# Kernel optimization log

Hardware: AMD Instinct MI355X
Metric: run time of the kernel (lower is better)

Reference implementation:

```python
import jax, jax.numpy as jnp
import numpy as np

V, E, H, OUT = 32000, 256, 256, 32000
B, TE, TD = 16, 128, 64


def gru_layer(x, h0, Wih, Whh, bih, bhh, lengths):
    """PyTorch-semantics GRU over padded batch-first x:(B,T,I), h0:(B,H).
    Emulates pack/pad: hidden frozen and output zeroed past each sample's length."""
    T = x.shape[1]

    def step(h, inp):
        xt, t = inp  # xt:(B,I)
        gi = xt @ Wih.T + bih          # (B,3H)
        gh = h @ Whh.T + bhh
        ir, iz, inn = jnp.split(gi, 3, axis=-1)
        hr, hz, hn = jnp.split(gh, 3, axis=-1)
        r = jax.nn.sigmoid(ir + hr)
        z = jax.nn.sigmoid(iz + hz)
        n = jnp.tanh(inn + r * hn)
        hnew = (1.0 - z) * n + z * h
        valid = (t < lengths)[:, None]
        h = jnp.where(valid, hnew, h)
        out = jnp.where(valid, hnew, 0.0)
        return h, out

    hT, ys = jax.lax.scan(step, h0, (jnp.swapaxes(x, 0, 1), jnp.arange(T)))
    return jnp.swapaxes(ys, 0, 1), hT  # (B,T,H), (B,H)


def setup_inputs() -> dict:
    key = jax.random.key(0)
    ks = jax.random.split(key, 20)
    s = 0.05
    enc_len = jax.random.randint(ks[0], (B,), 1, TE + 1).at[0].set(TE)
    dec_len = jax.random.randint(ks[1], (B,), 1, TD + 1).at[0].set(TD)
    return {
        "encoder_input": jax.random.randint(ks[2], (B, TE), 0, V),
        "encoder_length": enc_len,
        "decoder_input": jax.random.randint(ks[3], (B, TD), 0, V),
        "decoder_length": dec_len,
        "embedding": jax.random.normal(ks[4], (V, E)) * s,
        "enc_Wih": jax.random.normal(ks[5], (3 * H, E)) * s,
        "enc_Whh": jax.random.normal(ks[6], (3 * H, H)) * s,
        "enc_bih": jax.random.normal(ks[7], (3 * H,)) * s,
        "enc_bhh": jax.random.normal(ks[8], (3 * H,)) * s,
        "dec_Wih": jax.random.normal(ks[9], (3 * H, E)) * s,
        "dec_Whh": jax.random.normal(ks[10], (3 * H, H)) * s,
        "dec_bih": jax.random.normal(ks[11], (3 * H,)) * s,
        "dec_bhh": jax.random.normal(ks[12], (3 * H,)) * s,
        "attn_W": jax.random.normal(ks[13], (H, 2 * H)) * s,
        "attn_Wb": jnp.zeros((H,)),
        "attn_v": jax.random.normal(ks[14], (1, H)) * s,
        "attn_vb": jnp.zeros((1,)),
        "dense_W": jax.random.normal(ks[15], (H, 2 * H)) * s,
        "dense_b": jnp.zeros((H,)),
        "out_W": jax.random.normal(ks[16], (OUT, H)) * s,
        "out_b": jnp.zeros((OUT,)),
    }


def reference(encoder_input, encoder_length, decoder_input, decoder_length,
              embedding, enc_Wih, enc_Whh, enc_bih, enc_bhh,
              dec_Wih, dec_Whh, dec_bih, dec_bhh,
              attn_W, attn_Wb, attn_v, attn_vb,
              dense_W, dense_b, out_W, out_b):
    enc_x = embedding[encoder_input]  # (B,TE,E)
    dec_x = embedding[decoder_input]  # (B,TD,E)

    h0 = jnp.zeros((B, H), dtype=enc_x.dtype)
    enc_out, enc_h = gru_layer(enc_x, h0, enc_Wih, enc_Whh, enc_bih, enc_bhh, encoder_length)
    dec_out, _ = gru_layer(dec_x, enc_h, dec_Wih, dec_Whh, dec_bih, dec_bhh, decoder_length)

    # --- additive attention with per-sample length mask ---
    enc_valid = jnp.arange(TE) < encoder_length[:, None]     # (B,TE)
    dec_valid = jnp.arange(TD) < decoder_length[:, None]     # (B,TD)
    mask = (dec_valid[:, :, None] & enc_valid[:, None, :]).astype(enc_out.dtype)[..., None]  # (B,TD,TE,1)

    enc_e = enc_out[:, None, :, :] * mask  # (B,TD,TE,H)
    dec_e = dec_out[:, :, None, :] * mask  # (B,TD,TE,H)

    score = jnp.tanh(jnp.concatenate([enc_e, dec_e], axis=3) @ attn_W.T + attn_Wb)
    energy = score @ attn_v.T + attn_vb  # (B,TD,TE,1)
    a = jax.nn.softmax(energy, axis=2)   # softmax over encoder steps (unmasked, as original)
    aw = a * mask
    s = aw.sum(axis=2)                   # (B,TD,1)
    s = jnp.where(s == 0, 1.0, s)
    attention = aw / s[:, :, None, :]
    context = (attention * enc_e).sum(axis=2)  # (B,TD,H); dropout is identity (eval)

    outputs = jnp.concatenate([dec_out, context], axis=2)  # (B,TD,2H)
    dense = jnp.tanh(outputs @ dense_W.T + dense_b)
    logits = dense @ out_W.T + out_b  # (B,TD,OUT)
    return logits
```

## Files before the change

### kernel.cpp

```cpp
#include <hip/hip_runtime.h>
#include <hip/hip_bf16.h>

typedef unsigned short ushort_t;
typedef unsigned int uint_t;
typedef unsigned long long u64_t;

#define BB 16
#define TE 128
#define TD 64
#define HH 256
#define G3 768
#define KK 256
#define OUTV 32000
#define MROWS_E (BB*TE)
#define MROWS_D (BB*TD)
#define NBLK 16
#define JD 16
#define QW_PER_BUF 2048

typedef __attribute__((ext_vector_type(8))) short short8;
typedef __attribute__((ext_vector_type(4))) float f32x4;

__device__ __forceinline__ float b2f(ushort_t u) {
  union { uint_t i; float f; } v; v.i = ((uint_t)u) << 16; return v.f;
}
__device__ __forceinline__ ushort_t f2b(float f) {
  union { float f; uint_t i; } v; v.f = f;
  uint_t x = v.i;
  return (ushort_t)((x + 0x7fffu + ((x >> 16) & 1u)) >> 16);
}
__device__ __forceinline__ float ldf(const void* p, size_t i, uint_t f32f) {
  return f32f ? ((const float*)p)[i] : b2f(((const ushort_t*)p)[i]);
}
__device__ __forceinline__ float fsig(float x) { return 1.f/(1.f + __expf(-x)); }
__device__ __forceinline__ float ftanh(float x) { return 1.f - 2.f/(__expf(2.f*x) + 1.f); }

__global__ __launch_bounds__(256) void detect_kernel(const void* emb, uint_t* flag) {
  int tid = threadIdx.x;
  uint_t w = ((const uint_t*)emb)[tid];
  uint_t e = (w >> 7) & 0xFFu;
  bool pass = (e >= 100u && e <= 127u);
  unsigned long long m = __ballot(pass);
  __shared__ int cnt[4];
  if ((tid & 63) == 0) cnt[tid >> 6] = __popcll(m);
  __syncthreads();
  if (tid == 0) {
    int c = cnt[0] + cnt[1] + cnt[2] + cnt[3];
    *flag = (c >= 128) ? 0u : 1u;
  }
}

__global__ __launch_bounds__(256) void prep_kernel(
    const void* eWhh, const void* dWhh, const void* denseW,
    const void* ebih, const void* ebhh, const void* dbih, const void* dbhh,
    const void* outb, const uint_t* flagp,
    ushort_t* WBe, ushort_t* WBd, ushort_t* DWT,
    float* cbe, float* cbd, float* obf, u64_t* hq) {
  uint_t f = *flagp;
  int tid = blockIdx.x * blockDim.x + threadIdx.x;
  int nth = gridDim.x * blockDim.x;
  for (int i = tid; i < G3*KK; i += nth) {
    WBe[i] = f2b(ldf(eWhh, i, f));
    WBd[i] = f2b(ldf(dWhh, i, f));
  }
  for (int i = tid; i < 512*HH; i += nth) {
    int k = i / HH, c = i % HH;
    DWT[i] = f2b(ldf(denseW, (size_t)c*512 + k, f));
  }
  for (int i = tid; i < G3; i += nth) {
    float be = ldf(ebih, i, f), bd = ldf(dbih, i, f);
    if (i < 2*HH) { be += ldf(ebhh, i, f); bd += ldf(dbhh, i, f); }
    cbe[i] = be; cbd[i] = bd;
  }
  for (int i = tid; i < OUTV; i += nth) obf[i] = ldf(outb, i, f);
  for (int i = tid; i < 2*QW_PER_BUF; i += nth) hq[i] = 0ull;
}

#define LDT 264

__global__ __launch_bounds__(256) void gemm_kernel(
    const ushort_t* A, const int* tokens, const void* emb,
    const void* Bw, int ldb, int b_off,
    const float* bias, const uint_t* flagp,
    float* Cf, ushort_t* Cb, int ldc, int M, int tshift, int a_f32) {
  __shared__ __align__(16) ushort_t Bs[64*LDT];
  __shared__ __align__(16) ushort_t As[32*LDT];
  uint_t f = *flagp;
  int tid = threadIdx.x;
  int wave = tid >> 6, lane = tid & 63;
  int n0 = blockIdx.x * 64;
#pragma unroll
  for (int it = 0; it < 8; ++it) {
    int idx = it*256 + tid;
    int row = idx >> 5, col = (idx & 31) << 3;
    size_t e = (size_t)(n0 + row)*ldb + col + b_off;
    uint4 v;
    if (f) {
      const float4* s = (const float4*)((const float*)Bw + e);
      float4 x = s[0], y = s[1];
      v.x = (uint_t)f2b(x.x) | ((uint_t)f2b(x.y) << 16);
      v.y = (uint_t)f2b(x.z) | ((uint_t)f2b(x.w) << 16);
      v.z = (uint_t)f2b(y.x) | ((uint_t)f2b(y.y) << 16);
      v.w = (uint_t)f2b(y.z) | ((uint_t)f2b(y.w) << 16);
    } else {
      v = *(const uint4*)((const ushort_t*)Bw + e);
    }
    *(uint4*)(Bs + row*LDT + col) = v;
  }
  int arow_i = lane & 15;
  float bias_v = 0.f;
  if (bias) bias_v = bias[n0 + wave*16 + arow_i];
  int koff = (lane >> 4) << 3;
  for (int m0 = blockIdx.y*32; m0 < M; m0 += gridDim.y*32) {
    __syncthreads();
#pragma unroll
    for (int it = 0; it < 4; ++it) {
      int idx = it*256 + tid;
      int row = idx >> 5, col = (idx & 31) << 3;
      uint4 v;
      if (tokens) {
        size_t e = (size_t)tokens[m0 + row]*KK + col;
        if (f) {
          const float4* s = (const float4*)((const float*)emb + e);
          float4 x = s[0], y = s[1];
          v.x = (uint_t)f2b(x.x) | ((uint_t)f2b(x.y) << 16);
          v.y = (uint_t)f2b(x.z) | ((uint_t)f2b(x.w) << 16);
          v.z = (uint_t)f2b(y.x) | ((uint_t)f2b(y.y) << 16);
          v.w = (uint_t)f2b(y.z) | ((uint_t)f2b(y.w) << 16);
        } else {
          v = *(const uint4*)((const ushort_t*)emb + e);
        }
      } else if (a_f32) {
        const float4* s = (const float4*)((const float*)A + (size_t)(m0 + row)*KK + col);
        float4 x = s[0], y = s[1];
        v.x = (uint_t)f2b(x.x) | ((uint_t)f2b(x.y) << 16);
        v.y = (uint_t)f2b(x.z) | ((uint_t)f2b(x.w) << 16);
        v.z = (uint_t)f2b(y.x) | ((uint_t)f2b(y.y) << 16);
        v.w = (uint_t)f2b(y.z) | ((uint_t)f2b(y.w) << 16);
      } else {
        v = *(const uint4*)(A + (size_t)(m0 + row)*KK + col);
      }
      *(uint4*)(As + row*LDT + col) = v;
    }
    __syncthreads();
#pragma unroll
    for (int msub = 0; msub < 2; ++msub) {
      f32x4 acc = {0.f,0.f,0.f,0.f};
      const ushort_t* ap = As + (msub*16 + arow_i)*LDT + koff;
      const ushort_t* bp = Bs + (wave*16 + arow_i)*LDT + koff;
#pragma unroll
      for (int ks = 0; ks < 8; ++ks) {
        short8 af = *(const short8*)(ap + ks*32);
        short8 bf = *(const short8*)(bp + ks*32);
        acc = __builtin_amdgcn_mfma_f32_16x16x32_bf16(af, bf, acc, 0, 0, 0);
      }
      int mbase = m0 + msub*16 + (lane >> 4)*4;
      int ncol = n0 + wave*16 + arow_i;
#pragma unroll
      for (int r = 0; r < 4; ++r) {
        float val = acc[r] + bias_v;
        int mr = mbase + r;
        int orow = tshift ? (((mr & ((1 << tshift) - 1)) << 4) + (mr >> tshift)) : mr;
        if (Cf) Cf[(size_t)orow*ldc + ncol] = val;
        else    Cb[(size_t)orow*ldc + ncol] = f2b(val);
      }
    }
  }
}

#define HSBF 264

__device__ __forceinline__ void stage_w(const ushort_t* WB, int j0, int tid,
                                        ushort_t* wlds) {
#pragma unroll
  for (int it = 0; it < 6; ++it) {
    int idx = it*256 + tid;
    int row = idx >> 5, col = (idx & 31) << 3;
    const ushort_t* src = WB + ((size_t)((row >> 4)*HH + j0 + (row & 15)))*KK + col;
    *(uint4*)(wlds + row*HSBF + col) = *(const uint4*)src;
  }
}

__global__ __launch_bounds__(256) void gru_kernel(
    const float* gi_e, const float* gi_d, const ushort_t* WBe, const ushort_t* WBd,
    const void* ebhh, const void* dbhh, const uint_t* flagp,
    const int* elen, const int* dlen, float* eout, float* dout, u64_t* hq) {
  uint_t f = *flagp;
  __shared__ __align__(16) ushort_t wlds[48*HSBF];
  __shared__ __align__(16) float part[2][4][3][16][17];
  const int tid = threadIdx.x;
  const int wave = tid >> 6, lane = tid & 63;
  const int mrow = lane & 15, quad = lane >> 4;
  const int j0 = blockIdx.x * JD;
  const int m = tid >> 4, n = tid & 15;
  const int j = j0 + n;
  const int je = j & ~1;
  const int widx = ((je >> 6) << 9) + (((je >> 5) & 1) << 8)
                 + (((je >> 1) & 3) << 6) + (((je >> 3) & 3) << 4) + m;

  stage_w(WBe, j0, tid, wlds);
  const float bn_e = ldf(ebhh, 2*HH + j, f);
  const float bn_d = ldf(dbhh, 2*HH + j, f);
  const int len_e = elen[m], len_d = dlen[m];
  float hreg = 0.f;
  float grv = gi_e[(size_t)m*G3 + j];
  float gzv = gi_e[(size_t)m*G3 + HH + j];
  float gnv = gi_e[(size_t)m*G3 + 2*HH + j];
  __syncthreads();

  for (int s = 0; s < TE + TD; ++s) {
    if (s == TE) {
      stage_w(WBd, j0, tid, wlds);
      __syncthreads();
    }
    const bool enc = s < TE;
    const int t = enc ? s : s - TE;
    const u64_t* hbR = hq + (size_t)(s & 1)*QW_PER_BUF + wave*512 + lane;
    u64_t qv[8];
    const uint_t target = (uint_t)s;
    int guard = 0;
    for (;;) {
      bool ok = true;
#pragma unroll
      for (int ks = 0; ks < 2; ++ks)
#pragma unroll
        for (int i = 0; i < 4; ++i) {
          qv[ks*4 + i] = __hip_atomic_load(hbR + ks*256 + i*64,
                                           __ATOMIC_RELAXED, __HIP_MEMORY_SCOPE_AGENT);
          ok = ok && ((uint_t)qv[ks*4 + i] == target);
        }
      if (__all(ok) || ++guard > 30000) break;
    }
    f32x4 ar = {0.f,0.f,0.f,0.f}, az = {0.f,0.f,0.f,0.f}, an = {0.f,0.f,0.f,0.f};
#pragma unroll
    for (int ks = 0; ks < 2; ++ks) {
      union { uint_t u[4]; short8 s8; } av;
#pragma unroll
      for (int i = 0; i < 4; ++i) av.u[i] = (uint_t)(qv[ks*4 + i] >> 32);
      const ushort_t* wp = wlds + mrow*HSBF + wave*64 + ks*32 + quad*8;
      short8 b0 = *(const short8*)(wp);
      short8 b1 = *(const short8*)(wp + 16*HSBF);
      short8 b2 = *(const short8*)(wp + 32*HSBF);
      ar = __builtin_amdgcn_mfma_f32_16x16x32_bf16(av.s8, b0, ar, 0, 0, 0);
      az = __builtin_amdgcn_mfma_f32_16x16x32_bf16(av.s8, b1, az, 0, 0, 0);
      an = __builtin_amdgcn_mfma_f32_16x16x32_bf16(av.s8, b2, an, 0, 0, 0);
    }
    const int p = s & 1;
#pragma unroll
    for (int r = 0; r < 4; ++r) {
      part[p][wave][0][quad*4 + r][mrow] = ar[r];
      part[p][wave][1][quad*4 + r][mrow] = az[r];
      part[p][wave][2][quad*4 + r][mrow] = an[r];
    }
    __syncthreads();
    float accr = 0.f, accz = 0.f, accn = 0.f;
#pragma unroll
    for (int w = 0; w < 4; ++w) {
      accr += part[p][w][0][m][n];
      accz += part[p][w][1][m][n];
      accn += part[p][w][2][m][n];
    }
    float rr = fsig(grv + accr);
    float zz = fsig(gzv + accz);
    float nn = ftanh(gnv + rr*(accn + (enc ? bn_e : bn_d)));
    float hc = (1.f - zz)*nn + zz*hreg;
    bool valid = t < (enc ? len_e : len_d);
    float ov = valid ? hc : 0.f;
    hreg = valid ? hc : hreg;
    if (enc) eout[((size_t)(m*TE + t))*HH + j] = ov;
    else     dout[((size_t)(m*TD + t))*HH + j] = ov;
    uint_t h16 = (uint_t)f2b(hreg);
    uint_t up = (uint_t)__shfl_down((int)h16, 1);
    if (!(n & 1)) {
      u64_t q = ((u64_t)(h16 | (up << 16)) << 32) | (u64_t)(uint_t)(s + 1);
      __hip_atomic_store(hq + (size_t)((s + 1) & 1)*QW_PER_BUF + widx,
                         q, __ATOMIC_RELAXED, __HIP_MEMORY_SCOPE_AGENT);
    }
    int s2 = s + 1;
    if (s2 < TE + TD) {
      const float* g2 = (s2 < TE) ? (gi_e + (size_t)(s2*BB + m)*G3)
                                  : (gi_d + (size_t)((s2 - TE)*BB + m)*G3);
      grv = g2[j]; gzv = g2[HH + j]; gnv = g2[2*HH + j];
    }
  }
}

__global__ __launch_bounds__(256) void attn_kernel(
    const float* eprj, const float* dprj, const float* eout, const float* dout,
    const void* Wb, const void* av, const void* avb,
    const ushort_t* DWT, const void* db, const uint_t* flagp,
    const int* elen, const int* dlen, ushort_t* dense_bf) {
  int bd = blockIdx.x;
  int b = bd / TD, td = bd % TD;
  int tid = threadIdx.x;
  int wave = tid >> 6, lane = tid & 63;
  uint_t f = *flagp;
  __shared__ float dp[HH], dsrow[HH], vv[HH], att[TE];
  int el = elen[b];
  bool dok = td < dlen[b];
  size_t drow = (size_t)bd * HH;
  dp[tid] = dprj[drow + tid] + ldf(Wb, tid, f);
  dsrow[tid] = dout[drow + tid];
  vv[tid] = ldf(av, tid, f);
  if (tid < TE) att[tid] = 0.f;
  __syncthreads();
  float ctx = 0.f;
  if (dok) {
    float vb0 = ldf(avb, 0, f);
    int nteb = (el + 3) >> 2;
    for (int teb = 0; teb < nteb; ++teb) {
      int te = teb*4 + wave;
      if (te < el) {
        const float* ep = eprj + (size_t)(b*TE + te)*HH;
        float s = 0.f;
#pragma unroll
        for (int i = 0; i < 4; ++i) {
          int hh = lane + 64*i;
          s += ftanh(ep[hh] + dp[hh]) * vv[hh];
        }
#pragma unroll
        for (int off = 32; off > 0; off >>= 1) s += __shfl_xor(s, off);
        if (lane == 0) att[te] = s + vb0;
      }
    }
    __syncthreads();
    float mx = -1e30f;
    for (int te = 0; te < el; ++te) mx = fmaxf(mx, att[te]);
    __syncthreads();
    if (tid < el) att[tid] = __expf(att[tid] - mx);
    __syncthreads();
    float ssum = 0.f;
    for (int te = 0; te < el; ++te) ssum += att[te];
    float inv = (ssum > 0.f) ? 1.f/ssum : 0.f;
    const float* ebase = eout + (size_t)(b*TE)*HH + tid;
    float c0 = 0.f, c1 = 0.f, c2 = 0.f, c3 = 0.f;
    int te = 0;
    for (; te + 4 <= el; te += 4) {
      c0 += att[te    ] * ebase[(size_t)(te    )*HH];
      c1 += att[te + 1] * ebase[(size_t)(te + 1)*HH];
      c2 += att[te + 2] * ebase[(size_t)(te + 2)*HH];
      c3 += att[te + 3] * ebase[(size_t)(te + 3)*HH];
    }
    for (; te < el; ++te) c0 += att[te] * ebase[(size_t)te*HH];
    ctx = (c0 + c1 + c2 + c3) * inv;
  }
  __syncthreads();
  dp[tid] = ctx;
  __syncthreads();
  const ushort_t* w0 = DWT + tid;
  float a0 = ldf(db, tid, f), a1 = 0.f, a2 = 0.f, a3 = 0.f;
#pragma unroll 8
  for (int k = 0; k < HH; k += 4) {
    a0 = fmaf(b2f(w0[(size_t)(k    )*HH]), dsrow[k    ], a0);
    a1 = fmaf(b2f(w0[(size_t)(k + 1)*HH]), dsrow[k + 1], a1);
    a2 = fmaf(b2f(w0[(size_t)(k + 2)*HH]), dsrow[k + 2], a2);
    a3 = fmaf(b2f(w0[(size_t)(k + 3)*HH]), dsrow[k + 3], a3);
  }
#pragma unroll 8
  for (int k = 0; k < HH; k += 4) {
    a0 = fmaf(b2f(w0[(size_t)(HH + k    )*HH]), dp[k    ], a0);
    a1 = fmaf(b2f(w0[(size_t)(HH + k + 1)*HH]), dp[k + 1], a1);
    a2 = fmaf(b2f(w0[(size_t)(HH + k + 2)*HH]), dp[k + 2], a2);
    a3 = fmaf(b2f(w0[(size_t)(HH + k + 3)*HH]), dp[k + 3], a3);
  }
  dense_bf[drow + tid] = f2b(ftanh(a0 + a1 + a2 + a3));
}

extern "C" void kernel_launch(void* const* d_in, const int* in_sizes, int n_in,
                              void* d_out, int out_size, void* d_ws, size_t ws_size,
                              hipStream_t stream) {
  const int* enc_in   = (const int*)d_in[0];
  const int* enc_len  = (const int*)d_in[1];
  const int* dec_in   = (const int*)d_in[2];
  const int* dec_len  = (const int*)d_in[3];
  const void* emb    = d_in[4];
  const void* eWih   = d_in[5];
  const void* eWhh   = d_in[6];
  const void* ebih   = d_in[7];
  const void* ebhh   = d_in[8];
  const void* dWih   = d_in[9];
  const void* dWhh   = d_in[10];
  const void* dbih   = d_in[11];
  const void* dbhh   = d_in[12];
  const void* attnW  = d_in[13];
  const void* attnWb = d_in[14];
  const void* attnv  = d_in[15];
  const void* attnvb = d_in[16];
  const void* denseW = d_in[17];
  const void* denseb = d_in[18];
  const void* outW   = d_in[19];
  const void* outb   = d_in[20];
  float* out = (float*)d_out;

  float* ws = (float*)d_ws;
  size_t o = 0;
  uint_t* flag = (uint_t*)(ws + o);   o += 4;
  u64_t* hq = (u64_t*)(ws + o);       o += 4*QW_PER_BUF;
  ushort_t* WBe = (ushort_t*)(ws + o); o += G3*KK/2;
  ushort_t* WBd = (ushort_t*)(ws + o); o += G3*KK/2;
  ushort_t* DWT = (ushort_t*)(ws + o); o += 512*HH/2;
  float* cbe = ws + o;                o += G3;
  float* cbd = ws + o;                o += G3;
  float* obf = ws + o;                o += OUTV;
  float* gi_e = ws + o;               o += (size_t)MROWS_E*G3;
  float* gi_d = ws + o;               o += (size_t)MROWS_D*G3;
  float* eout = ws + o;               o += (size_t)MROWS_E*HH;
  float* dout = ws + o;               o += (size_t)MROWS_D*HH;
  float* eprj = ws + o;               o += (size_t)MROWS_E*HH;
  float* dprj = ws + o;               o += (size_t)MROWS_D*HH;
  ushort_t* dense_bf = (ushort_t*)(ws + o); o += (size_t)MROWS_D*HH/2;

  detect_kernel<<<1, 256, 0, stream>>>(emb, flag);
  prep_kernel<<<384, 256, 0, stream>>>(eWhh, dWhh, denseW, ebih, ebhh, dbih, dbhh,
                                       outb, flag, WBe, WBd, DWT, cbe, cbd, obf, hq);
  gemm_kernel<<<dim3(12,8), 256, 0, stream>>>(nullptr, enc_in, emb, eWih, 256, 0,
                                              cbe, flag, gi_e, nullptr, G3, MROWS_E, 7, 0);
  gemm_kernel<<<dim3(12,4), 256, 0, stream>>>(nullptr, dec_in, emb, dWih, 256, 0,
                                              cbd, flag, gi_d, nullptr, G3, MROWS_D, 6, 0);
  gru_kernel<<<NBLK, 256, 0, stream>>>(gi_e, gi_d, WBe, WBd, ebhh, dbhh, flag,
                                       enc_len, dec_len, eout, dout, hq);
  gemm_kernel<<<dim3(4,16), 256, 0, stream>>>((const ushort_t*)eout, nullptr, nullptr,
                                              attnW, 512, 0, nullptr, flag, eprj,
                                              nullptr, HH, MROWS_E, 0, 1);
  gemm_kernel<<<dim3(4,8), 256, 0, stream>>>((const ushort_t*)dout, nullptr, nullptr,
                                             attnW, 512, 256, nullptr, flag, dprj,
                                             nullptr, HH, MROWS_D, 0, 1);
  attn_kernel<<<MROWS_D, 256, 0, stream>>>(eprj, dprj, eout, dout, attnWb, attnv, attnvb,
                                           DWT, denseb, flag, enc_len, dec_len, dense_bf);
  gemm_kernel<<<dim3(500,4), 256, 0, stream>>>(dense_bf, nullptr, nullptr, outW, 256, 0,
                                               obf, flag, out, nullptr, OUTV, MROWS_D, 0, 0);
}
```

Baseline: 743.6 us.

## Shrink GRU recurrence to four blocks with 64 hidden columns each

Repartitions the persistent GRU recurrence from 16 blocks of 16 hidden units to 4 blocks of 64 units. Each block now stages a 192-row weight slice in LDS and does 12 MFMAs per k-step per wave. Each thread updates four hidden units with float4 loads and stores. The point is to cut the number of blocks taking part in the cross-block flag-polling handshake at every timestep, since that handshake dominates the latency-bound recurrence. The cost is more per-block compute and LDS per step, a reworked h-exchange layout, and an extra __syncthreads per step in place of the double-buffered partials.

```diff
diff --git a/kernel.cpp b/kernel.cpp
--- a/kernel.cpp
+++ b/kernel.cpp
@@ -14,8 +14,9 @@
 #define OUTV 32000
 #define MROWS_E (BB*TE)
 #define MROWS_D (BB*TD)
-#define NBLK 16
-#define JD 16
+#define NBLK 4
+#define JD 64
+#define WROWS 192
 #define QW_PER_BUF 2048
 
 typedef __attribute__((ext_vector_type(8))) short short8;
@@ -173,10 +174,10 @@
 __device__ __forceinline__ void stage_w(const ushort_t* WB, int j0, int tid,
                                         ushort_t* wlds) {
 #pragma unroll
-  for (int it = 0; it < 6; ++it) {
+  for (int it = 0; it < 24; ++it) {
     int idx = it*256 + tid;
     int row = idx >> 5, col = (idx & 31) << 3;
-    const ushort_t* src = WB + ((size_t)((row >> 4)*HH + j0 + (row & 15)))*KK + col;
+    const ushort_t* src = WB + ((size_t)((row >> 6)*HH + j0 + (row & 63)))*KK + col;
     *(uint4*)(wlds + row*HSBF + col) = *(const uint4*)src;
   }
 }
@@ -186,26 +187,32 @@
     const void* ebhh, const void* dbhh, const uint_t* flagp,
     const int* elen, const int* dlen, float* eout, float* dout, u64_t* hq) {
   uint_t f = *flagp;
-  __shared__ __align__(16) ushort_t wlds[48*HSBF];
-  __shared__ __align__(16) float part[2][4][3][16][17];
+  __shared__ __align__(16) ushort_t wlds[WROWS*HSBF];
+  __shared__ __align__(16) float part[4][12][16][17];
   const int tid = threadIdx.x;
   const int wave = tid >> 6, lane = tid & 63;
   const int mrow = lane & 15, quad = lane >> 4;
-  const int j0 = blockIdx.x * JD;
-  const int m = tid >> 4, n = tid & 15;
-  const int j = j0 + n;
-  const int je = j & ~1;
-  const int widx = ((je >> 6) << 9) + (((je >> 5) & 1) << 8)
-                 + (((je >> 1) & 3) << 6) + (((je >> 3) & 3) << 4) + m;
+  const int bid = blockIdx.x;
+  const int j0 = bid * JD;
+  const int m = tid >> 4, g = tid & 15;
+  const int jb = 4*g;
+  const int pl0 = 2*g, pl1 = 2*g + 1;
+  const int widx0 = bid*512 + (pl0 >> 4)*256 + ((pl0 >> 2) & 3)*64 + (pl0 & 3)*16 + m;
+  const int widx1 = bid*512 + (pl1 >> 4)*256 + ((pl1 >> 2) & 3)*64 + (pl1 & 3)*16 + m;
 
   stage_w(WBe, j0, tid, wlds);
-  const float bn_e = ldf(ebhh, 2*HH + j, f);
-  const float bn_d = ldf(dbhh, 2*HH + j, f);
+  float bn_e[4], bn_d[4];
+#pragma unroll
+  for (int d = 0; d < 4; ++d) {
+    bn_e[d] = ldf(ebhh, 2*HH + j0 + jb + d, f);
+    bn_d[d] = ldf(dbhh, 2*HH + j0 + jb + d, f);
+  }
   const int len_e = elen[m], len_d = dlen[m];
-  float hreg = 0.f;
-  float grv = gi_e[(size_t)m*G3 + j];
-  float gzv = gi_e[(size_t)m*G3 + HH + j];
-  float gnv = gi_e[(size_t)m*G3 + 2*HH + j];
+  float hreg[4] = {0.f, 0.f, 0.f, 0.f};
+  const float* g0p = gi_e + (size_t)m*G3;
+  float4 gr = *(const float4*)(g0p + j0 + jb);
+  float4 gz = *(const float4*)(g0p + HH + j0 + jb);
+  float4 gn = *(const float4*)(g0p + 2*HH + j0 + jb);
   __syncthreads();
 
   for (int s = 0; s < TE + TD; ++s) {
@@ -215,7 +222,7 @@
     }
     const bool enc = s < TE;
     const int t = enc ? s : s - TE;
-    const u64_t* hbR = hq + (size_t)(s & 1)*QW_PER_BUF + wave*512 + lane;
+    const u64_t* hbR = hq + (size_t)(s & 1)*QW_PER_BUF + wave*512 + quad*64 + mrow;
     u64_t qv[8];
     const uint_t target = (uint_t)s;
     int guard = 0;
@@ -224,64 +231,79 @@
 #pragma unroll
       for (int ks = 0; ks < 2; ++ks)
 #pragma unroll
-        for (int i = 0; i < 4; ++i) {
-          qv[ks*4 + i] = __hip_atomic_load(hbR + ks*256 + i*64,
+        for (int e = 0; e < 4; ++e) {
+          qv[ks*4 + e] = __hip_atomic_load(hbR + ks*256 + e*16,
                                            __ATOMIC_RELAXED, __HIP_MEMORY_SCOPE_AGENT);
-          ok = ok && ((uint_t)qv[ks*4 + i] == target);
+          ok = ok && ((uint_t)qv[ks*4 + e] == target);
         }
       if (__all(ok) || ++guard > 30000) break;
     }
-    f32x4 ar = {0.f,0.f,0.f,0.f}, az = {0.f,0.f,0.f,0.f}, an = {0.f,0.f,0.f,0.f};
+    f32x4 acc[3][4];
+#pragma unroll
+    for (int ga = 0; ga < 3; ++ga)
+#pragma unroll
+      for (int jt = 0; jt < 4; ++jt) acc[ga][jt] = (f32x4){0.f,0.f,0.f,0.f};
 #pragma unroll
     for (int ks = 0; ks < 2; ++ks) {
       union { uint_t u[4]; short8 s8; } av;
 #pragma unroll
-      for (int i = 0; i < 4; ++i) av.u[i] = (uint_t)(qv[ks*4 + i] >> 32);
-      const ushort_t* wp = wlds + mrow*HSBF + wave*64 + ks*32 + quad*8;
-      short8 b0 = *(const short8*)(wp);
-      short8 b1 = *(const short8*)(wp + 16*HSBF);
-      short8 b2 = *(const short8*)(wp + 32*HSBF);
-      ar = __builtin_amdgcn_mfma_f32_16x16x32_bf16(av.s8, b0, ar, 0, 0, 0);
-      az = __builtin_amdgcn_mfma_f32_16x16x32_bf16(av.s8, b1, az, 0, 0, 0);
-      an = __builtin_amdgcn_mfma_f32_16x16x32_bf16(av.s8, b2, an, 0, 0, 0);
-    }
-    const int p = s & 1;
-#pragma unroll
-    for (int r = 0; r < 4; ++r) {
-      part[p][wave][0][quad*4 + r][mrow] = ar[r];
-      part[p][wave][1][quad*4 + r][mrow] = az[r];
-      part[p][wave][2][quad*4 + r][mrow] = an[r];
-    }
-    __syncthreads();
-    float accr = 0.f, accz = 0.f, accn = 0.f;
-#pragma unroll
-    for (int w = 0; w < 4; ++w) {
-      accr += part[p][w][0][m][n];
-      accz += part[p][w][1][m][n];
-      accn += part[p][w][2][m][n];
-    }
-    float rr = fsig(grv + accr);
-    float zz = fsig(gzv + accz);
-    float nn = ftanh(gnv + rr*(accn + (enc ? bn_e : bn_d)));
-    float hc = (1.f - zz)*nn + zz*hreg;
-    bool valid = t < (enc ? len_e : len_d);
-    float ov = valid ? hc : 0.f;
-    hreg = valid ? hc : hreg;
-    if (enc) eout[((size_t)(m*TE + t))*HH + j] = ov;
-    else     dout[((size_t)(m*TD + t))*HH + j] = ov;
-    uint_t h16 = (uint_t)f2b(hreg);
-    uint_t up = (uint_t)__shfl_down((int)h16, 1);
-    if (!(n & 1)) {
-      u64_t q = ((u64_t)(h16 | (up << 16)) << 32) | (u64_t)(uint_t)(s + 1);
-      __hip_atomic_store(hq + (size_t)((s + 1) & 1)*QW_PER_BUF + widx,
-                         q, __ATOMIC_RELAXED, __HIP_MEMORY_SCOPE_AGENT);
-    }
+      for (int e = 0; e < 4; ++e) av.u[e] = (uint_t)(qv[ks*4 + e] >> 32);
+      const ushort_t* wb = wlds + mrow*HSBF + wave*64 + ks*32 + quad*8;
+#pragma unroll
+      for (int ga = 0; ga < 3; ++ga)
+#pragma unroll
+        for (int jt = 0; jt < 4; ++jt) {
+          short8 bv = *(const short8*)(wb + (ga*64 + jt*16)*HSBF);
+          acc[ga][jt] = __builtin_amdgcn_mfma_f32_16x16x32_bf16(av.s8, bv, acc[ga][jt], 0, 0, 0);
+        }
+    }
+#pragma unroll
+    for (int ga = 0; ga < 3; ++ga)
+#pragma unroll
+      for (int jt = 0; jt < 4; ++jt)
+#pragma unroll
+        for (int r = 0; r < 4; ++r)
+          part[wave][ga*4 + jt][quad*4 + r][mrow] = acc[ga][jt][r];
+    __syncthreads();
+    const int ttj = g >> 2, cb = (g & 3)*4;
+    const int len = enc ? len_e : len_d;
+    const bool valid = t < len;
+    float h4[4];
+#pragma unroll
+    for (int d = 0; d < 4; ++d) {
+      float ar = 0.f, az = 0.f, an = 0.f;
+#pragma unroll
+      for (int w = 0; w < 4; ++w) {
+        ar += part[w][ttj    ][m][cb + d];
+        az += part[w][4 + ttj][m][cb + d];
+        an += part[w][8 + ttj][m][cb + d];
+      }
+      float rr = fsig(gr[d] + ar);
+      float zz = fsig(gz[d] + az);
+      float nn = ftanh(gn[d] + rr*(an + (enc ? bn_e[d] : bn_d[d])));
+      float hc = (1.f - zz)*nn + zz*hreg[d];
+      h4[d] = valid ? hc : 0.f;
+      hreg[d] = valid ? hc : hreg[d];
+    }
+    float4 ov4 = {h4[0], h4[1], h4[2], h4[3]};
+    if (enc) *(float4*)(eout + ((size_t)(m*TE + t))*HH + j0 + jb) = ov4;
+    else     *(float4*)(dout + ((size_t)(m*TD + t))*HH + j0 + jb) = ov4;
+    uint_t q0 = (uint_t)f2b(hreg[0]) | ((uint_t)f2b(hreg[1]) << 16);
+    uint_t q1 = (uint_t)f2b(hreg[2]) | ((uint_t)f2b(hreg[3]) << 16);
+    u64_t* hbW = hq + (size_t)((s + 1) & 1)*QW_PER_BUF;
+    __hip_atomic_store(hbW + widx0, ((u64_t)q0 << 32) | (u64_t)(uint_t)(s + 1),
+                       __ATOMIC_RELAXED, __HIP_MEMORY_SCOPE_AGENT);
+    __hip_atomic_store(hbW + widx1, ((u64_t)q1 << 32) | (u64_t)(uint_t)(s + 1),
+                       __ATOMIC_RELAXED, __HIP_MEMORY_SCOPE_AGENT);
     int s2 = s + 1;
     if (s2 < TE + TD) {
       const float* g2 = (s2 < TE) ? (gi_e + (size_t)(s2*BB + m)*G3)
                                   : (gi_d + (size_t)((s2 - TE)*BB + m)*G3);
-      grv = g2[j]; gzv = g2[HH + j]; gnv = g2[2*HH + j];
-    }
+      gr = *(const float4*)(g2 + j0 + jb);
+      gz = *(const float4*)(g2 + HH + j0 + jb);
+      gn = *(const float4*)(g2 + 2*HH + j0 + jb);
+    }
+    __syncthreads();
   }
 }
 
```

Result: slower. 934.9 us (+25.7%).
